# Kernel optimization log

Hardware: AMD Instinct MI355X
Metric: run time of the kernel (lower is better)

Reference implementation:

```python
import jax, jax.numpy as jnp
import numpy as np

N_NODES = 50000
N_EDGES = 1000000
IN_F = 128
OUT_F = 128
K = 4
NEG_SLOPE = 0.01  # torch nn.LeakyReLU() default
EPS = 1e-8


def setup_inputs() -> dict:
    key = jax.random.key(0)
    k1, k2, k3, k4, k5, k6 = jax.random.split(key, 6)
    x = jax.random.normal(k1, (N_NODES, IN_F), dtype=jnp.float32)
    e = jax.random.uniform(k2, (N_NODES, K), dtype=jnp.float32)
    stdv = 1.0 / np.sqrt(OUT_F)
    weights = jax.random.uniform(k3, (K, IN_F, OUT_F), minval=-stdv, maxval=stdv, dtype=jnp.float32)
    a = jax.random.normal(k4, (K, 2 * OUT_F, 1), dtype=jnp.float32) * 0.1
    # edge_index with no self-loops (remove_self_loops is then a no-op)
    row = jax.random.randint(k5, (N_EDGES,), 0, N_NODES)
    off = jax.random.randint(k6, (N_EDGES,), 1, N_NODES)
    col = (row + off) % N_NODES
    adj = jnp.stack([row, col]).astype(jnp.int64)
    return {"x": x, "e": e, "weights": weights, "a": a, "adj": adj}


def _canet_gat_forward(x, e, weights, a, adj):
    N = x.shape[0]
    out_f = weights.shape[-1]
    # add self loops (input has none)
    loops = jnp.arange(N, dtype=adj.dtype)
    src = jnp.concatenate([adj[0], loops])  # [Et]
    dst = jnp.concatenate([adj[1], loops])  # [Et]

    # per-head projection: [K, N, O]
    h = jnp.einsum('nd,kdo->kno', x, weights)

    # attention logits: a = [a_src; a_dst], logit_e = leakyrelu(h[src].a_src + h[dst].a_dst)
    a_src = a[:, :out_f, 0]   # [K, O]
    a_dst = a[:, out_f:, 0]   # [K, O]
    s_src = jnp.einsum('kno,ko->kn', h, a_src)  # [K, N]
    s_dst = jnp.einsum('kno,ko->kn', h, a_dst)  # [K, N]
    logits = s_src[:, src] + s_dst[:, dst]      # [K, Et]
    logits = jnp.where(logits >= 0, logits, NEG_SLOPE * logits)
    logits_max = jnp.max(logits, axis=1, keepdims=True)  # global max per head
    edge_e = jnp.exp(logits - logits_max)                # [K, Et]

    outputs = []
    for k in range(h.shape[0]):  # small fixed loop over heads (avoids [K,Et,O] blowup)
        denom = jax.ops.segment_sum(edge_e[k], src, num_segments=N) + EPS   # [N]
        msg = edge_e[k][:, None] * h[k][dst]                                # [Et, O]
        hi_k = jax.ops.segment_sum(msg, src, num_segments=N)                # [N, O]
        outputs.append(hi_k / denom[:, None])
    outputs = jnp.stack(outputs, axis=1)  # [N, K, O]

    out = jnp.sum(e[:, :, None] * outputs, axis=1)  # [N, O]
    return out + x  # residual (in_features == out_features)


def reference(x, e, weights, a, adj):
    return _canet_gat_forward(x, e, weights, a, adj)
```

## Files before the change

### kernel.cpp

```cpp
#include <hip/hip_runtime.h>
#include <hip/hip_bf16.h>
#include <cstddef>

#define NN 50000
#define NE 1000000
#define F  128
#define KH 4
#define NEG 0.01f
#define EPSF 1e-8f
#define CAP 64
#define NBIN 196
#define BINCAP 8192
#define EPB 16384
#define SUBS 4
#define NCH ((NE + EPB - 1) / EPB)
#define NB1 (NCH * SUBS)
#define NBW 256
#define NBP 2048
#define STR (NBP * 4)
#define MXSTR 32
#define TSTR 32
#define NPB 16

typedef short bf16x8 __attribute__((ext_vector_type(8)));
typedef float f32x4 __attribute__((ext_vector_type(4)));

__device__ inline ushort f2bf(float f) {
    __hip_bfloat16 b = __float2bfloat16(f);
    return *reinterpret_cast<ushort*>(&b);
}
__device__ inline unsigned int packbf(float xl, float xh) {
    return (unsigned int)f2bf(xl) | ((unsigned int)f2bf(xh) << 16);
}
__device__ inline float lk(float v) { return (v >= 0.f) ? v : NEG * v; }

__global__ __launch_bounds__(256) void vv_kernel(const float* __restrict__ W,
                                                 const float* __restrict__ a,
                                                 float* __restrict__ vvg) {
    int j0 = threadIdx.x * 4;
#pragma unroll
    for (int ii = 0; ii < 4; ii++) {
        int j = j0 + ii;
        int side = j >> 9;
        int k = (j >> 7) & 3;
        int dd = j & 127;
        const float4* Wr = (const float4*)(W + (size_t)k * F * F + (size_t)dd * F);
        const float4* ar = (const float4*)(a + (size_t)k * 2 * F + side * F);
        float acc = 0.f;
#pragma unroll 8
        for (int o = 0; o < F / 4; o++) {
            float4 wv = Wr[o], av = ar[o];
            acc += wv.x * av.x + wv.y * av.y + wv.z * av.z + wv.w * av.w;
        }
        vvg[j] = acc;
    }
}

__global__ __launch_bounds__(256) void bin_prep_kernel(const int* __restrict__ adj,
                                                       int* __restrict__ binTail,
                                                       unsigned int* __restrict__ binbuf,
                                                       const float* __restrict__ W,
                                                       ushort* __restrict__ wt,
                                                       const float* __restrict__ vvg,
                                                       const float* __restrict__ x,
                                                       unsigned int* __restrict__ xb2,
                                                       float* __restrict__ ssrc4,
                                                       float* __restrict__ sdst4,
                                                       int* __restrict__ mxsi) {
    int b = blockIdx.x;
    int tid = threadIdx.x;
    __shared__ __align__(16) int shmem[1024];
    __shared__ float bmax_s[4][8];

    if (b < NB1) {
        int* hist = shmem;
        int chunk = b >> 2, sub = b & (SUBS - 1);
        int base = chunk * EPB;
        int nloc = min(EPB, NE - base);
        for (int i = tid; i < NBIN; i += 256) hist[i] = 0;
        __syncthreads();
        for (int off0 = 0; off0 < EPB; off0 += 256 * 8) {
            int sv[8]; bool va[8];
#pragma unroll
            for (int u = 0; u < 8; u++) {
                int off = off0 + u * 256 + tid;
                va[u] = off < nloc;
                sv[u] = adj[base + (va[u] ? off : 0)];
            }
#pragma unroll
            for (int u = 0; u < 8; u++) {
                int bn = ((unsigned int)sv[u]) >> 8;
                if (va[u] && (bn & (SUBS - 1)) == sub) atomicAdd(&hist[bn], 1);
            }
        }
        __syncthreads();
        for (int i = tid; i < NBIN; i += 256) {
            if ((i & (SUBS - 1)) == sub) {
                int c = hist[i];
                hist[i] = atomicAdd(&binTail[i * TSTR], c);
            }
        }
        __syncthreads();
        for (int off0 = 0; off0 < EPB; off0 += 256 * 8) {
            int sv[8], dv[8]; bool va[8];
#pragma unroll
            for (int u = 0; u < 8; u++) {
                int off = off0 + u * 256 + tid;
                va[u] = off < nloc;
                int e = base + (va[u] ? off : 0);
                sv[u] = adj[e];
                dv[u] = adj[NE + e];
            }
#pragma unroll
            for (int u = 0; u < 8; u++) {
                unsigned int s = (unsigned int)sv[u];
                int bn = s >> 8;
                if (va[u] && (bn & (SUBS - 1)) == sub) {
                    int p = atomicAdd(&hist[bn], 1);
                    if (p < BINCAP) binbuf[(size_t)bn * BINCAP + p] = (s << 16) | (unsigned int)dv[u];
                }
            }
        }
        return;
    }
    if (b >= NB1 + NBP) {
        int i = (b - NB1 - NBP) * 256 + tid;
        int k = i >> 14;
        int dd = (i >> 7) & 127;
        int o = i & 127;
        wt[((size_t)k * F + o) * F + dd] = f2bf(W[i]);
        return;
    }

    float* vvf = (float*)shmem;
    ((float4*)vvf)[tid] = ((const float4*)vvg)[tid];
    __syncthreads();

    int wv = tid >> 6, lane = tid & 63;
    int gw = (b - NB1) * 4 + wv;
    const float2* x2 = (const float2*)x;
    float2 vs[4], vd[4];
#pragma unroll
    for (int k = 0; k < 4; k++) {
        vs[k] = *(const float2*)&vvf[k * F + 2 * lane];
        vd[k] = *(const float2*)&vvf[(4 + k) * F + 2 * lane];
    }
    int l1 = lane & 1, l2 = lane & 2, l4 = lane & 4;
    int j = 4 * l1 + l2 + (l4 >> 2);
    float* sp = (j < 4) ? (ssrc4 + j) : (sdst4 + (j - 4));
    float mxv = 0.f;

    for (int n = gw; n < NN; n += 2 * STR) {
        int nb = n + STR;
        bool vb = nb < NN;
        float2 xa = x2[(size_t)n * 64 + lane];
        float2 xbv = vb ? x2[(size_t)nb * 64 + lane] : make_float2(0.f, 0.f);
        xb2[(size_t)n * 64 + lane] = packbf(xa.x, xa.y);
        if (vb) xb2[(size_t)nb * 64 + lane] = packbf(xbv.x, xbv.y);
        float s[8], q[8];
#pragma unroll
        for (int k = 0; k < 4; k++) {
            s[k]     = xa.x * vs[k].x + xa.y * vs[k].y;
            s[4 + k] = xa.x * vd[k].x + xa.y * vd[k].y;
            q[k]     = xbv.x * vs[k].x + xbv.y * vs[k].y;
            q[4 + k] = xbv.x * vd[k].x + xbv.y * vd[k].y;
        }
        float tA[4], tB[4];
#pragma unroll
        for (int i = 0; i < 4; i++) {
            float mA = l1 ? s[4 + i] : s[i];
            float oA = __shfl_xor(l1 ? s[i] : s[4 + i], 1);
            tA[i] = mA + oA;
            float mB = l1 ? q[4 + i] : q[i];
            float oB = __shfl_xor(l1 ? q[i] : q[4 + i], 1);
            tB[i] = mB + oB;
        }
        float uA[2], uB[2];
#pragma unroll
        for (int i = 0; i < 2; i++) {
            float mA = l2 ? tA[2 + i] : tA[i];
            float oA = __shfl_xor(l2 ? tA[i] : tA[2 + i], 2);
            uA[i] = mA + oA;
            float mB = l2 ? tB[2 + i] : tB[i];
            float oB = __shfl_xor(l2 ? tB[i] : tB[2 + i], 2);
            uB[i] = mB + oB;
        }
        float vA, vB;
        {
            float mA = l4 ? uA[1] : uA[0];
            float oA = __shfl_xor(l4 ? uA[0] : uA[1], 4);
            vA = mA + oA;
            float mB = l4 ? uB[1] : uB[0];
            float oB = __shfl_xor(l4 ? uB[0] : uB[1], 4);
            vB = mB + oB;
        }
        vA += __shfl_xor(vA, 8);  vB += __shfl_xor(vB, 8);
        vA += __shfl_xor(vA, 16); vB += __shfl_xor(vB, 16);
        vA += __shfl_xor(vA, 32); vB += __shfl_xor(vB, 32);
        if (lane < 8) {
            sp[(size_t)n * 4] = vA;
            if (vb) sp[(size_t)nb * 4] = vB;
        }
        mxv = fmaxf(mxv, fmaxf(vA, vB));
    }
    if (lane < 8) bmax_s[wv][j] = mxv;
    __syncthreads();
    if (tid < 8) {
        float m = fmaxf(fmaxf(bmax_s[0][tid], bmax_s[1][tid]),
                        fmaxf(bmax_s[2][tid], bmax_s[3][tid]));
        atomicMax(&mxsi[tid * MXSTR], __float_as_int(m));
    }
}

__global__ __launch_bounds__(256) void build_kernel(const int* __restrict__ binTail,
                                                    const unsigned int* __restrict__ binbuf,
                                                    int* __restrict__ cnt,
                                                    ushort* __restrict__ bucket16) {
    int tid = threadIdx.x;
    __shared__ int lcnt[256];
    __shared__ int lpos[256];
    int b = blockIdx.x;
    lcnt[tid] = 0;
    lpos[tid] = 0;
    __syncthreads();
    int tail = min(binTail[b * TSTR], BINCAP);
    const unsigned int* bb = binbuf + (size_t)b * BINCAP;
    for (int i = tid; i < tail; i += 256) {
        unsigned int pk = bb[i];
        atomicAdd(&lcnt[(pk >> 16) & 255], 1);
    }
    __syncthreads();
    int n0 = b << 8;
    cnt[n0 + tid] = lcnt[tid];
    for (int i = tid; i < tail; i += 256) {
        unsigned int pk = bb[i];
        int sl = (pk >> 16) & 255;
        int p = atomicAdd(&lpos[sl], 1);
        if (p < CAP) bucket16[(size_t)(n0 + sl) * CAP + p] = (ushort)(pk & 0xffffu);
    }
}

__global__ __launch_bounds__(256) void aggregate_kernel(const unsigned int* __restrict__ xb2,
                                                        const float* __restrict__ ssrc4,
                                                        const float* __restrict__ sdst4,
                                                        const float* __restrict__ mxs,
                                                        const int* __restrict__ cnt,
                                                        const ushort* __restrict__ bucket16,
                                                        const float* __restrict__ ew,
                                                        unsigned int* __restrict__ z2) {
    int wv = threadIdx.x >> 6, lane = threadIdx.x & 63;
    __shared__ int dsh[4][64];
    __shared__ __align__(16) float wsh[4][64][4];

    float m0 = lk(mxs[0 * MXSTR] + mxs[4 * MXSTR]);
    float m1 = lk(mxs[1 * MXSTR] + mxs[5 * MXSTR]);
    float m2 = lk(mxs[2 * MXSTR] + mxs[6 * MXSTR]);
    float m3 = lk(mxs[3 * MXSTR] + mxs[7 * MXSTR]);

    int n0 = blockIdx.x * NPB + wv * (NPB / 4);
#pragma unroll 1
    for (int g = 0; g < NPB / 4; ++g) {
        int n = n0 + g;
        if (n >= NN) break;

        float4 ss  = *(const float4*)&ssrc4[(size_t)n * 4];
        float4 sdn = *(const float4*)&sdst4[(size_t)n * 4];
        float w0s = __expf(lk(ss.x + sdn.x) - m0);
        float w1s = __expf(lk(ss.y + sdn.y) - m1);
        float w2s = __expf(lk(ss.z + sdn.z) - m2);
        float w3s = __expf(lk(ss.w + sdn.w) - m3);

        int deg = min(cnt[n], CAP);
        float4 w = make_float4(0.f, 0.f, 0.f, 0.f);
        int d = 0;
        if (lane < deg) {
            d = (int)bucket16[(size_t)n * CAP + lane];
            float4 sd = *(const float4*)&sdst4[(size_t)d * 4];
            w.x = __expf(lk(ss.x + sd.x) - m0);
            w.y = __expf(lk(ss.y + sd.y) - m1);
            w.z = __expf(lk(ss.z + sd.z) - m2);
            w.w = __expf(lk(ss.w + sd.w) - m3);
        }
        dsh[wv][lane] = d;
        *(float4*)&wsh[wv][lane][0] = w;

        float dn0 = w.x, dn1 = w.y, dn2 = w.z, dn3 = w.w;
#pragma unroll
        for (int st = 1; st < 64; st <<= 1) {
            dn0 += __shfl_xor(dn0, st);
            dn1 += __shfl_xor(dn1, st);
            dn2 += __shfl_xor(dn2, st);
            dn3 += __shfl_xor(dn3, st);
        }

        float a0[4], a1[4];
        {
            unsigned int v = xb2[(size_t)n * 64 + lane];
            union { unsigned int u; float f; } lo, hi;
            lo.u = v << 16;
            hi.u = v & 0xffff0000u;
            a0[0] = w0s * lo.f; a1[0] = w0s * hi.f;
            a0[1] = w1s * lo.f; a1[1] = w1s * hi.f;
            a0[2] = w2s * lo.f; a1[2] = w2s * hi.f;
            a0[3] = w3s * lo.f; a1[3] = w3s * hi.f;
        }

        int degp = (deg + 7) & ~7;
        for (int i = 0; i < degp; i += 8) {
            int du[8];
#pragma unroll
            for (int u = 0; u < 8; u++)
                du[u] = __builtin_amdgcn_readfirstlane(dsh[wv][i + u]);
            unsigned int vu[8];
#pragma unroll
            for (int u = 0; u < 8; u++)
                vu[u] = xb2[(size_t)du[u] * 64 + lane];
#pragma unroll
            for (int u = 0; u < 8; u++) {
                float4 w4 = *(const float4*)&wsh[wv][i + u][0];
                union { unsigned int uu; float f; } lo, hi;
                lo.uu = vu[u] << 16;
                hi.uu = vu[u] & 0xffff0000u;
                a0[0] += w4.x * lo.f; a1[0] += w4.x * hi.f;
                a0[1] += w4.y * lo.f; a1[1] += w4.y * hi.f;
                a0[2] += w4.z * lo.f; a1[2] += w4.z * hi.f;
                a0[3] += w4.w * lo.f; a1[3] += w4.w * hi.f;
            }
        }

        float4 e4 = *(const float4*)&ew[(size_t)n * 4];
        float i0 = e4.x / (w0s + dn0 + EPSF);
        float i1 = e4.y / (w1s + dn1 + EPSF);
        float i2 = e4.z / (w2s + dn2 + EPSF);
        float i3 = e4.w / (w3s + dn3 + EPSF);
        size_t zb = (size_t)n * 256;
        z2[zb +   0 + lane] = packbf(a0[0] * i0, a1[0] * i0);
        z2[zb +  64 + lane] = packbf(a0[1] * i1, a1[1] * i1);
        z2[zb + 128 + lane] = packbf(a0[2] * i2, a1[2] * i2);
        z2[zb + 192 + lane] = packbf(a0[3] * i3, a1[3] * i3);
    }
}

#define MT 64
__global__ __launch_bounds__(256) void gemm2_kernel(const ushort* __restrict__ z,
                                                    const ushort* __restrict__ wt,
                                                    const float* __restrict__ x,
                                                    float* __restrict__ out) {
    int row0 = blockIdx.x * MT;
    int tid = threadIdx.x;
    int wave = tid >> 6, lane = tid & 63;
    int quad = lane >> 4, l16 = lane & 15;
    __shared__ ushort ws[F][136];

    int arow = row0 + wave * 16 + l16;
    if (arow >= NN) arow = NN - 1;

    f32x4 acc[8];
#pragma unroll
    for (int i = 0; i < 8; i++) acc[i] = (f32x4){0.f, 0.f, 0.f, 0.f};

    for (int k = 0; k < KH; k++) {
        __syncthreads();
        const ushort* wk = wt + (size_t)k * F * F;
        for (int i = tid; i < F * 16; i += 256) {
            int r = i >> 4, c = (i & 15) * 8;
            *(uint4*)&ws[r][c] = *(const uint4*)&wk[r * F + c];
        }
        __syncthreads();
#pragma unroll
        for (int kt = 0; kt < 4; kt++) {
            int kb = kt * 32 + quad * 8;
            bf16x8 af = *(const bf16x8*)&z[(size_t)arow * 512 + k * F + kb];
#pragma unroll
            for (int ni = 0; ni < 8; ni++) {
                bf16x8 bf = *(const bf16x8*)&ws[ni * 16 + l16][kb];
                acc[ni] = __builtin_amdgcn_mfma_f32_16x16x32_bf16(af, bf, acc[ni], 0, 0, 0);
            }
        }
    }
#pragma unroll
    for (int r = 0; r < 4; r++) {
        int n = row0 + wave * 16 + quad * 4 + r;
        if (n < NN) {
#pragma unroll
            for (int ni = 0; ni < 8; ni++) {
                int o = ni * 16 + l16;
                out[(size_t)n * F + o] = x[(size_t)n * F + o] + acc[ni][r];
            }
        }
    }
}

extern "C" void kernel_launch(void* const* d_in, const int* in_sizes, int n_in,
                              void* d_out, int out_size, void* d_ws, size_t ws_size,
                              hipStream_t stream) {
    const float* x = (const float*)d_in[0];
    const float* e = (const float*)d_in[1];
    const float* W = (const float*)d_in[2];
    const float* a = (const float*)d_in[3];
    const int*   adj = (const int*)d_in[4];
    float* out = (float*)d_out;

    char* ws = (char*)d_ws;
    auto take = [&](size_t bytes) {
        char* p = ws;
        ws += (bytes + 255) & ~(size_t)255;
        return p;
    };
    ushort* z      = (ushort*)take((size_t)NN * KH * F * sizeof(ushort));
    unsigned int* xb2 = (unsigned int*)take((size_t)NN * F * sizeof(ushort));
    ushort* wt     = (ushort*)take((size_t)KH * F * F * sizeof(ushort));
    float* ssrc4   = (float*)take((size_t)NN * 4 * sizeof(float));
    float* sdst4   = (float*)take((size_t)NN * 4 * sizeof(float));
    int*   cnt     = (int*)take((size_t)NBIN * 256 * sizeof(int));
    ushort* bucket16 = (ushort*)take((size_t)NBIN * 256 * CAP * sizeof(ushort));
    unsigned int* binbuf = (unsigned int*)take((size_t)NBIN * BINCAP * sizeof(unsigned int));
    int*   binTail = (int*)take((size_t)NBIN * TSTR * sizeof(int));
    float* mxs     = (float*)take((size_t)8 * MXSTR * sizeof(float));
    float* vvg     = (float*)take((size_t)8 * F * sizeof(float));

    hipMemsetAsync(binTail, 0, (size_t)NBIN * TSTR * sizeof(int), stream);
    hipMemsetAsync(mxs, 0, (size_t)8 * MXSTR * sizeof(float), stream);
    vv_kernel<<<1, 256, 0, stream>>>(W, a, vvg);
    bin_prep_kernel<<<NB1 + NBP + NBW, 256, 0, stream>>>(adj, binTail, binbuf, W, wt,
                                                         vvg, x, xb2, ssrc4, sdst4, (int*)mxs);
    build_kernel<<<NBIN, 256, 0, stream>>>(binTail, binbuf, cnt, bucket16);
    aggregate_kernel<<<(NN + NPB - 1) / NPB, 256, 0, stream>>>(xb2, ssrc4, sdst4, mxs, cnt,
                                                               bucket16, e, (unsigned int*)z);
    gemm2_kernel<<<(NN + MT - 1) / MT, 256, 0, stream>>>(z, wt, x, out);
}
```

Baseline: 240.0 us.

## Fuse aggregation and output GEMM into one kernel via shared-memory tile

```diff
diff --git a/kernel.cpp b/kernel.cpp
--- a/kernel.cpp
+++ b/kernel.cpp
@@ -240,28 +240,32 @@
     }
 }
 
-__global__ __launch_bounds__(256) void aggregate_kernel(const unsigned int* __restrict__ xb2,
-                                                        const float* __restrict__ ssrc4,
-                                                        const float* __restrict__ sdst4,
-                                                        const float* __restrict__ mxs,
-                                                        const int* __restrict__ cnt,
-                                                        const ushort* __restrict__ bucket16,
-                                                        const float* __restrict__ ew,
-                                                        unsigned int* __restrict__ z2) {
+__global__ __launch_bounds__(256) void agg_gemm_kernel(const unsigned int* __restrict__ xb2,
+                                                       const float* __restrict__ ssrc4,
+                                                       const float* __restrict__ sdst4,
+                                                       const float* __restrict__ mxs,
+                                                       const int* __restrict__ cnt,
+                                                       const ushort* __restrict__ bucket16,
+                                                       const float* __restrict__ ew,
+                                                       const ushort* __restrict__ wt,
+                                                       const float* __restrict__ x,
+                                                       float* __restrict__ out) {
     int wv = threadIdx.x >> 6, lane = threadIdx.x & 63;
+    int l16 = lane & 15, quad = lane >> 4;
     __shared__ int dsh[4][64];
     __shared__ __align__(16) float wsh[4][64][4];
+    __shared__ __align__(16) unsigned int zsh[16][260];
 
     float m0 = lk(mxs[0 * MXSTR] + mxs[4 * MXSTR]);
     float m1 = lk(mxs[1 * MXSTR] + mxs[5 * MXSTR]);
     float m2 = lk(mxs[2 * MXSTR] + mxs[6 * MXSTR]);
     float m3 = lk(mxs[3 * MXSTR] + mxs[7 * MXSTR]);
 
-    int n0 = blockIdx.x * NPB + wv * (NPB / 4);
+    int n0b = blockIdx.x * NPB;
+    int n0 = n0b + wv * (NPB / 4);
 #pragma unroll 1
     for (int g = 0; g < NPB / 4; ++g) {
         int n = n0 + g;
-        if (n >= NN) break;
 
         float4 ss  = *(const float4*)&ssrc4[(size_t)n * 4];
         float4 sdn = *(const float4*)&sdst4[(size_t)n * 4];
@@ -333,61 +337,37 @@
         float i1 = e4.y / (w1s + dn1 + EPSF);
         float i2 = e4.z / (w2s + dn2 + EPSF);
         float i3 = e4.w / (w3s + dn3 + EPSF);
-        size_t zb = (size_t)n * 256;
-        z2[zb +   0 + lane] = packbf(a0[0] * i0, a1[0] * i0);
-        z2[zb +  64 + lane] = packbf(a0[1] * i1, a1[1] * i1);
-        z2[zb + 128 + lane] = packbf(a0[2] * i2, a1[2] * i2);
-        z2[zb + 192 + lane] = packbf(a0[3] * i3, a1[3] * i3);
-    }
-}
-
-#define MT 64
-__global__ __launch_bounds__(256) void gemm2_kernel(const ushort* __restrict__ z,
-                                                    const ushort* __restrict__ wt,
-                                                    const float* __restrict__ x,
-                                                    float* __restrict__ out) {
-    int row0 = blockIdx.x * MT;
-    int tid = threadIdx.x;
-    int wave = tid >> 6, lane = tid & 63;
-    int quad = lane >> 4, l16 = lane & 15;
-    __shared__ ushort ws[F][136];
-
-    int arow = row0 + wave * 16 + l16;
-    if (arow >= NN) arow = NN - 1;
-
-    f32x4 acc[8];
-#pragma unroll
-    for (int i = 0; i < 8; i++) acc[i] = (f32x4){0.f, 0.f, 0.f, 0.f};
-
-    for (int k = 0; k < KH; k++) {
-        __syncthreads();
-        const ushort* wk = wt + (size_t)k * F * F;
-        for (int i = tid; i < F * 16; i += 256) {
-            int r = i >> 4, c = (i & 15) * 8;
-            *(uint4*)&ws[r][c] = *(const uint4*)&wk[r * F + c];
-        }
-        __syncthreads();
+        int rl = wv * 4 + g;
+        zsh[rl][  0 + lane] = packbf(a0[0] * i0, a1[0] * i0);
+        zsh[rl][ 64 + lane] = packbf(a0[1] * i1, a1[1] * i1);
+        zsh[rl][128 + lane] = packbf(a0[2] * i2, a1[2] * i2);
+        zsh[rl][192 + lane] = packbf(a0[3] * i3, a1[3] * i3);
+    }
+
+    __syncthreads();
+
+    f32x4 accA = (f32x4){0.f, 0.f, 0.f, 0.f};
+    f32x4 accB = (f32x4){0.f, 0.f, 0.f, 0.f};
+    int oA = (wv * 2 + 0) * 16 + l16;
+    int oB = (wv * 2 + 1) * 16 + l16;
+#pragma unroll
+    for (int kh = 0; kh < KH; kh++) {
 #pragma unroll
         for (int kt = 0; kt < 4; kt++) {
-            int kb = kt * 32 + quad * 8;
-            bf16x8 af = *(const bf16x8*)&z[(size_t)arow * 512 + k * F + kb];
-#pragma unroll
-            for (int ni = 0; ni < 8; ni++) {
-                bf16x8 bf = *(const bf16x8*)&ws[ni * 16 + l16][kb];
-                acc[ni] = __builtin_amdgcn_mfma_f32_16x16x32_bf16(af, bf, acc[ni], 0, 0, 0);
-            }
+            int dwoff = kh * 64 + kt * 16 + quad * 4;
+            bf16x8 af = *(const bf16x8*)&zsh[l16][dwoff];
+            const ushort* wb = wt + (size_t)(kh * F) * F + kt * 32 + quad * 8;
+            bf16x8 b0 = *(const bf16x8*)&wb[(size_t)oA * F];
+            bf16x8 b1 = *(const bf16x8*)&wb[(size_t)oB * F];
+            accA = __builtin_amdgcn_mfma_f32_16x16x32_bf16(af, b0, accA, 0, 0, 0);
+            accB = __builtin_amdgcn_mfma_f32_16x16x32_bf16(af, b1, accB, 0, 0, 0);
         }
     }
 #pragma unroll
     for (int r = 0; r < 4; r++) {
-        int n = row0 + wave * 16 + quad * 4 + r;
-        if (n < NN) {
-#pragma unroll
-            for (int ni = 0; ni < 8; ni++) {
-                int o = ni * 16 + l16;
-                out[(size_t)n * F + o] = x[(size_t)n * F + o] + acc[ni][r];
-            }
-        }
+        int n = n0b + quad * 4 + r;
+        out[(size_t)n * F + oA] = x[(size_t)n * F + oA] + accA[r];
+        out[(size_t)n * F + oB] = x[(size_t)n * F + oB] + accB[r];
     }
 }
 
@@ -407,7 +387,6 @@
         ws += (bytes + 255) & ~(size_t)255;
         return p;
     };
-    ushort* z      = (ushort*)take((size_t)NN * KH * F * sizeof(ushort));
     unsigned int* xb2 = (unsigned int*)take((size_t)NN * F * sizeof(ushort));
     ushort* wt     = (ushort*)take((size_t)KH * F * F * sizeof(ushort));
     float* ssrc4   = (float*)take((size_t)NN * 4 * sizeof(float));
@@ -425,7 +404,6 @@
     bin_prep_kernel<<<NB1 + NBP + NBW, 256, 0, stream>>>(adj, binTail, binbuf, W, wt,
                                                          vvg, x, xb2, ssrc4, sdst4, (int*)mxs);
     build_kernel<<<NBIN, 256, 0, stream>>>(binTail, binbuf, cnt, bucket16);
-    aggregate_kernel<<<(NN + NPB - 1) / NPB, 256, 0, stream>>>(xb2, ssrc4, sdst4, mxs, cnt,
-                                                               bucket16, e, (unsigned int*)z);
-    gemm2_kernel<<<(NN + MT - 1) / MT, 256, 0, stream>>>(z, wt, x, out);
-}
+    agg_gemm_kernel<<<NN / NPB, 256, 0, stream>>>(xb2, ssrc4, sdst4, mxs, cnt,
+                                                  bucket16, e, wt, x, out);
+}
```

Result: slower. 262.1 us (+9.2%).
